# Kernel optimization log

Measured on AMD Instinct MI355X. Metric: run time of the kernel, lower is better.

## Reference

```python
import jax, jax.numpy as jnp
import numpy as np
from jax import lax

N = 200000
CIN = 64
COUT = 128
K = 27  # 3^3 kernel offsets
EPS = 1e-5


def _make_rulebook(key, n, k):
    ki, km = jax.random.split(key)
    idx = jax.random.randint(ki, (k, n), 0, n, dtype=jnp.int32)
    keep = jax.random.uniform(km, (k, n)) < 0.5
    idx = jnp.where(keep, idx, -1)
    # center offset is always the voxel itself (submanifold conv)
    idx = idx.at[k // 2].set(jnp.arange(n, dtype=jnp.int32))
    return idx


def setup_inputs() -> dict:
    key = jax.random.key(0)
    ks = jax.random.split(key, 8)
    feats = jax.random.normal(ks[0], (N, CIN), dtype=jnp.float32)
    nbr1 = _make_rulebook(ks[1], N, K)
    nbr2 = _make_rulebook(ks[2], N, K)
    W1 = jax.random.normal(ks[3], (K, CIN, COUT), dtype=jnp.float32) * 0.05
    W2 = jax.random.normal(ks[4], (K, COUT, COUT), dtype=jnp.float32) * 0.05
    Wd = jax.random.normal(ks[5], (CIN, COUT), dtype=jnp.float32) * 0.05
    g1 = jnp.ones((COUT,), jnp.float32); b1 = jnp.zeros((COUT,), jnp.float32)
    g2 = jnp.ones((COUT,), jnp.float32); b2 = jnp.zeros((COUT,), jnp.float32)
    gd = jnp.ones((COUT,), jnp.float32); bd = jnp.zeros((COUT,), jnp.float32)
    return dict(feats=feats, nbr1=nbr1, nbr2=nbr2, W1=W1, W2=W2, Wd=Wd,
                g1=g1, b1=b1, g2=g2, b2=b2, gd=gd, bd=bd)


def sparse_conv(feats, W, nbr):
    """Rulebook sparse conv: gather neighbors per offset, GEMM, accumulate.
    feats: [N, Cin]; W: [K, Cin, Cout]; nbr: [K, N] int (-1 = missing)."""
    n = feats.shape[0]
    acc0 = jnp.zeros((n, W.shape[-1]), feats.dtype)

    def body(acc, xs):
        idx, Wk = xs  # [N], [Cin, Cout]
        valid = (idx >= 0).astype(feats.dtype)[:, None]
        g = feats[jnp.clip(idx, 0)] * valid  # masked gather [N, Cin]
        return acc + g @ Wk, None

    out, _ = lax.scan(body, acc0, (nbr, W))
    return out


def batchnorm(x, gamma, beta):
    mean = jnp.mean(x, axis=0)
    var = jnp.var(x, axis=0)
    return (x - mean) * lax.rsqrt(var + EPS) * gamma + beta


def reference(feats, nbr1, nbr2, W1, W2, Wd, g1, b1, g2, b2, gd, bd):
    h = sparse_conv(feats, W1, nbr1)
    h = jax.nn.relu(batchnorm(h, g1, b1))
    h = sparse_conv(h, W2, nbr2)
    h = batchnorm(h, g2, b2)
    skip = batchnorm(feats @ Wd, gd, bd)  # 1x1 conv downsample (Cin != Cout)
    return jax.nn.relu(h + skip)
```

## Files before the change

### kernel.cpp

```cpp
#include <hip/hip_runtime.h>
#include <stdint.h>

#define KOFF 27
#define CIN 64
#define COUT 128
#define EPS 1e-5f

using frag_ab = __attribute__((ext_vector_type(8))) short;
using frag_cd = __attribute__((ext_vector_type(4))) float;

__device__ __forceinline__ float bf2f(unsigned short u) {
  union { unsigned int i; float f; } x; x.i = ((unsigned int)u) << 16; return x.f;
}
__device__ __forceinline__ unsigned short f2bf(float f) {
  union { float f; unsigned int i; } x; x.f = f;
  unsigned int u = x.i;
  u += 0x7fffu + ((u >> 16) & 1u);
  return (unsigned short)(u >> 16);
}

__device__ __forceinline__ void gld16(const void* gptr, void* lptr) {
  __builtin_amdgcn_global_load_lds(
      (const __attribute__((address_space(1))) unsigned int*)gptr,
      (__attribute__((address_space(3))) unsigned int*)lptr, 16, 0, 0);
}

template <int CI, bool GATHER, bool OF32>
__global__ __launch_bounds__(256, 3) void conv_kernel(
    const unsigned short* __restrict__ X, const int* __restrict__ nbr,
    const unsigned short* __restrict__ Wt, void* __restrict__ Yv,
    const unsigned short* __restrict__ zpage, float* __restrict__ sums,
    int n, int koff) {
  constexpr int NC = CI / 32;
  __shared__ unsigned short Alds[3][128 * 32];

  const int tid = threadIdx.x;
  const int lane = tid & 63;
  const int wave = tid >> 6;
  const int row0 = blockIdx.x * 128;
  const int wrow = (wave >> 1) * 64;
  const int wcol = (wave & 1) * 64;
  const int m = lane & 15;
  const int q = lane >> 4;
  const int srow0 = wave * 16 + (lane >> 2);
  const int sl = lane & 3;

  frag_cd acc[4][4];
#pragma unroll
  for (int i = 0; i < 4; ++i)
#pragma unroll
    for (int j = 0; j < 4; ++j) acc[i][j] = (frag_cd){0.f, 0.f, 0.f, 0.f};

  frag_ab bA[4], bB[4];
  int idxc[2], idxn[2];

  auto load_idx = [&](int ko, int (&dst)[2]) {
#pragma unroll
    for (int i = 0; i < 2; ++i) {
      const int grow = row0 + srow0 + i * 64;
      int v = -1;
      if (grow < n) v = GATHER ? nbr[(size_t)ko * n + grow] : grow;
      dst[i] = v;
    }
  };
  auto stageA = [&](int buf, int ko, int kc, const int (&idx)[2]) {
#pragma unroll
    for (int i = 0; i < 2; ++i) {
      const int row = srow0 + i * 64;
      const int g = sl ^ ((row >> 1) & 3);
      const unsigned short* ga =
          (idx[i] >= 0) ? X + (size_t)idx[i] * CI + kc * 32 + g * 8 : zpage;
      gld16(ga, &Alds[buf][(i * 64 + wave * 16) * 32]);
    }
  };
  auto loadB = [&](frag_ab (&b)[4], int ko, int kc) {
    const unsigned short* base =
        Wt + (size_t)(ko * NC + kc) * 4096 + q * 1024 + m * 8;
#pragma unroll
    for (int j = 0; j < 4; ++j)
      b[j] = *(const frag_ab*)(base + (wcol + 16 * j) * 8);
  };
  auto do_mfma = [&](int buf, frag_ab (&b)[4]) {
    frag_ab a[4];
#pragma unroll
    for (int i = 0; i < 4; ++i) {
      const int row = wrow + 16 * i + m;
      a[i] = *(const frag_ab*)(&Alds[buf][row * 32 + (q ^ ((row >> 1) & 3)) * 8]);
    }
#pragma unroll
    for (int i = 0; i < 4; ++i)
#pragma unroll
      for (int j = 0; j < 4; ++j)
        acc[i][j] = __builtin_amdgcn_mfma_f32_16x16x32_bf16(a[i], b[j],
                                                            acc[i][j], 0, 0, 0);
  };

  const int T = koff * NC;
  load_idx(0, idxc);
  if (koff > 1) load_idx(1, idxn);
  stageA(0, 0, 0, idxc);
  stageA(1, 0, 1, idxc);
  loadB(bA, 0, 0);

  int bufc = 0;
  auto body = [&](int t, frag_ab (&bcur)[4], frag_ab (&bnxt)[4]) {
    asm volatile("s_waitcnt vmcnt(6)" ::: "memory");
    __builtin_amdgcn_s_barrier();
    const int s = t + 2;
    if (s < T && GATHER) {
      const int kos = s / NC;
      if ((s & (NC - 1)) == 0) {
        idxc[0] = idxn[0];
        idxc[1] = idxn[1];
        if (kos + 1 < koff) load_idx(kos + 1, idxn);
      }
    }
    const int u = t + 1;
    if (u < T) loadB(bnxt, u / NC, u & (NC - 1));
    if (s < T) {
      int bufs = bufc + 2; if (bufs >= 3) bufs -= 3;
      stageA(bufs, s / NC, s & (NC - 1), idxc);
    }
    do_mfma(bufc, bcur);
    if (++bufc == 3) bufc = 0;
  };

  for (int t = 0; t + 3 < T; t += 2) {
    body(t, bA, bB);
    body(t + 1, bB, bA);
  }
  body(T - 2, bA, bB);
  asm volatile("s_waitcnt vmcnt(0)" ::: "memory");
  __builtin_amdgcn_s_barrier();
  do_mfma(bufc, bB);

#pragma unroll
  for (int j = 0; j < 4; ++j) {
    float s = 0.f, qq = 0.f;
#pragma unroll
    for (int i = 0; i < 4; ++i)
#pragma unroll
      for (int r = 0; r < 4; ++r) {
        float v = acc[i][j][r];
        s += v; qq += v * v;
      }
    s += __shfl_xor(s, 16); s += __shfl_xor(s, 32);
    qq += __shfl_xor(qq, 16); qq += __shfl_xor(qq, 32);
    if (lane < 16) {
      const int col = wcol + 16 * j + lane;
      atomicAdd(&sums[col], s);
      atomicAdd(&sums[COUT + col], qq);
    }
  }

#pragma unroll
  for (int i = 0; i < 4; ++i) {
#pragma unroll
    for (int r = 0; r < 4; ++r) {
      const int grow = row0 + wrow + 16 * i + q * 4 + r;
      if (grow < n) {
#pragma unroll
        for (int j = 0; j < 4; ++j) {
          const int gcol = wcol + 16 * j + m;
          if (OF32)
            ((float*)Yv)[(size_t)grow * COUT + gcol] = acc[i][j][r];
          else
            ((unsigned short*)Yv)[(size_t)grow * COUT + gcol] = f2bf(acc[i][j][r]);
        }
      }
    }
  }
}

__global__ __launch_bounds__(256, 2) void convskip_kernel(
    const float* __restrict__ feats, const float* __restrict__ Wd,
    unsigned short* __restrict__ featsb, unsigned short* __restrict__ sX,
    float* __restrict__ sums, int n) {
  __shared__ unsigned short Alds[2][128 * 32];
  const int tid = threadIdx.x;
  const int lane = tid & 63;
  const int wave = tid >> 6;
  const int row0 = blockIdx.x * 128;
  const int wrow = (wave >> 1) * 64;
  const int wcol = (wave & 1) * 64;
  const int m = lane & 15;
  const int q = lane >> 4;

#pragma unroll
  for (int c = 0; c < 4; ++c) {
    int u = c * 256 + tid;
    int kc = u >> 9;
    int v = u & 511;
    int row = v >> 2;
    int s = v & 3;
    int g = s ^ ((row >> 1) & 3);
    int grow = row0 + row;
    uint4 out = make_uint4(0u, 0u, 0u, 0u);
    if (grow < n) {
      const float* p = feats + (size_t)grow * 64 + kc * 32 + g * 8;
      float4 lo = *(const float4*)p;
      float4 hi = *(const float4*)(p + 4);
      out.x = (unsigned)f2bf(lo.x) | ((unsigned)f2bf(lo.y) << 16);
      out.y = (unsigned)f2bf(lo.z) | ((unsigned)f2bf(lo.w) << 16);
      out.z = (unsigned)f2bf(hi.x) | ((unsigned)f2bf(hi.y) << 16);
      out.w = (unsigned)f2bf(hi.z) | ((unsigned)f2bf(hi.w) << 16);
      *(uint4*)(featsb + (size_t)grow * 64 + kc * 32 + g * 8) = out;
    }
    *(uint4*)(&Alds[kc][row * 32 + s * 8]) = out;
  }
  __syncthreads();

  frag_cd acc[4][4];
#pragma unroll
  for (int i = 0; i < 4; ++i)
#pragma unroll
    for (int j = 0; j < 4; ++j) acc[i][j] = (frag_cd){0.f, 0.f, 0.f, 0.f};

#pragma unroll
  for (int kc = 0; kc < 2; ++kc) {
    frag_ab b[4];
#pragma unroll
    for (int j = 0; j < 4; ++j) {
      const int co = wcol + 16 * j + m;
#pragma unroll
      for (int e = 0; e < 8; ++e)
        b[j][e] = (short)f2bf(Wd[(size_t)(kc * 32 + q * 8 + e) * 128 + co]);
    }
    frag_ab a[4];
#pragma unroll
    for (int i = 0; i < 4; ++i) {
      const int row = wrow + 16 * i + m;
      a[i] = *(const frag_ab*)(&Alds[kc][row * 32 + (q ^ ((row >> 1) & 3)) * 8]);
    }
#pragma unroll
    for (int i = 0; i < 4; ++i)
#pragma unroll
      for (int j = 0; j < 4; ++j)
        acc[i][j] = __builtin_amdgcn_mfma_f32_16x16x32_bf16(a[i], b[j],
                                                            acc[i][j], 0, 0, 0);
  }

#pragma unroll
  for (int j = 0; j < 4; ++j) {
    float s = 0.f, qq = 0.f;
#pragma unroll
    for (int i = 0; i < 4; ++i)
#pragma unroll
      for (int r = 0; r < 4; ++r) {
        float v = acc[i][j][r];
        s += v; qq += v * v;
      }
    s += __shfl_xor(s, 16); s += __shfl_xor(s, 32);
    qq += __shfl_xor(qq, 16); qq += __shfl_xor(qq, 32);
    if (lane < 16) {
      const int col = wcol + 16 * j + lane;
      atomicAdd(&sums[col], s);
      atomicAdd(&sums[COUT + col], qq);
    }
  }

#pragma unroll
  for (int i = 0; i < 4; ++i) {
#pragma unroll
    for (int r = 0; r < 4; ++r) {
      const int grow = row0 + wrow + 16 * i + q * 4 + r;
      if (grow < n) {
#pragma unroll
        for (int j = 0; j < 4; ++j)
          sX[(size_t)grow * COUT + wcol + 16 * j + m] = f2bf(acc[i][j][r]);
      }
    }
  }
}

__global__ void prep_kernel(const float* __restrict__ W1,
                            const float* __restrict__ W2,
                            unsigned short* __restrict__ Wt1,
                            unsigned short* __restrict__ Wt2,
                            float* __restrict__ zbase,
                            float* __restrict__ zpage) {
  const int NZ = 768 + 64;
  const int NW1 = KOFF * CIN * 128;
  const int NW2 = KOFF * COUT * 128;
  int gid = blockIdx.x * 256 + threadIdx.x;
  if (gid < NZ) {
    if (gid < 768) zbase[gid] = 0.f; else zpage[gid - 768] = 0.f;
    return;
  }
  gid -= NZ;
  const float* src;
  unsigned short* dst;
  int ci;
  if (gid < NW1) { src = W1; dst = Wt1; ci = CIN; }
  else if (gid < NW1 + NW2) { gid -= NW1; src = W2; dst = Wt2; ci = COUT; }
  else return;
  int e = gid & 7;
  int co = (gid >> 3) & 127;
  int qq = (gid >> 10) & 3;
  int slab = gid >> 12;
  int nc = ci >> 5;
  int ko = slab / nc;
  int kc = slab - ko * nc;
  int cin = kc * 32 + qq * 8 + e;
  dst[gid] = f2bf(src[((size_t)ko * ci + cin) * 128 + co]);
}

__global__ void norm_relu_kernel(unsigned short* __restrict__ x,
                                 const float* __restrict__ sums,
                                 const float* __restrict__ gamma,
                                 const float* __restrict__ beta,
                                 int n, int total8) {
  __shared__ float sc[COUT], sh[COUT];
  const int tid = threadIdx.x;
  if (tid < COUT) {
    float inv_n = 1.f / (float)n;
    float mean = sums[tid] * inv_n;
    float var = sums[COUT + tid] * inv_n - mean * mean;
    float s = gamma[tid] * rsqrtf(var + EPS);
    sc[tid] = s;
    sh[tid] = beta[tid] - mean * s;
  }
  __syncthreads();
  int gid = blockIdx.x * 256 + tid;
  if (gid >= total8) return;
  size_t i = (size_t)gid * 8;
  int c0 = (int)(i & 127);
  uint4 v = *(const uint4*)(x + i);
  unsigned int w[4] = {v.x, v.y, v.z, v.w};
  unsigned int wo[4];
#pragma unroll
  for (int e = 0; e < 4; ++e) {
    int c = c0 + 2 * e;
    float f0 = bf2f((unsigned short)(w[e] & 0xffffu));
    float f1 = bf2f((unsigned short)(w[e] >> 16));
    f0 = fmaxf(f0 * sc[c] + sh[c], 0.f);
    f1 = fmaxf(f1 * sc[c + 1] + sh[c + 1], 0.f);
    wo[e] = (unsigned int)f2bf(f0) | ((unsigned int)f2bf(f1) << 16);
  }
  *(uint4*)(x + i) = make_uint4(wo[0], wo[1], wo[2], wo[3]);
}

__global__ void final_kernel(float* __restrict__ h2,
                             const unsigned short* __restrict__ s,
                             const float* __restrict__ sums2,
                             const float* __restrict__ sumsd,
                             const float* __restrict__ g2,
                             const float* __restrict__ b2,
                             const float* __restrict__ gd,
                             const float* __restrict__ bd,
                             int n, int total4) {
  __shared__ float sc2[COUT], sh2[COUT], scd[COUT], shd[COUT];
  const int tid = threadIdx.x;
  if (tid < COUT) {
    float inv_n = 1.f / (float)n;
    float mean = sums2[tid] * inv_n;
    float var = sums2[COUT + tid] * inv_n - mean * mean;
    float sa = g2[tid] * rsqrtf(var + EPS);
    sc2[tid] = sa;
    sh2[tid] = b2[tid] - mean * sa;
    mean = sumsd[tid] * inv_n;
    var = sumsd[COUT + tid] * inv_n - mean * mean;
    float sb = gd[tid] * rsqrtf(var + EPS);
    scd[tid] = sb;
    shd[tid] = bd[tid] - mean * sb;
  }
  __syncthreads();
  int gid = blockIdx.x * 256 + tid;
  if (gid >= total4) return;
  size_t i = (size_t)gid * 4;
  int c = (int)(i & 127);
  float4 a = *(const float4*)(h2 + i);
  uint2 sv = *(const uint2*)(s + i);
  float b0 = bf2f((unsigned short)(sv.x & 0xffffu));
  float b1 = bf2f((unsigned short)(sv.x >> 16));
  float b2f = bf2f((unsigned short)(sv.y & 0xffffu));
  float b3 = bf2f((unsigned short)(sv.y >> 16));
  float4 o;
  o.x = fmaxf(a.x * sc2[c] + sh2[c] + b0 * scd[c] + shd[c], 0.f);
  o.y = fmaxf(a.y * sc2[c + 1] + sh2[c + 1] + b1 * scd[c + 1] + shd[c + 1], 0.f);
  o.z = fmaxf(a.z * sc2[c + 2] + sh2[c + 2] + b2f * scd[c + 2] + shd[c + 2], 0.f);
  o.w = fmaxf(a.w * sc2[c + 3] + sh2[c + 3] + b3 * scd[c + 3] + shd[c + 3], 0.f);
  *(float4*)(h2 + i) = o;
}

extern "C" void kernel_launch(void* const* d_in, const int* in_sizes, int n_in,
                              void* d_out, int out_size, void* d_ws,
                              size_t ws_size, hipStream_t stream) {
  (void)n_in; (void)out_size; (void)ws_size;
  const float* feats = (const float*)d_in[0];
  const int* nbr1 = (const int*)d_in[1];
  const int* nbr2 = (const int*)d_in[2];
  const float* W1 = (const float*)d_in[3];
  const float* W2 = (const float*)d_in[4];
  const float* Wd = (const float*)d_in[5];
  const float* g1 = (const float*)d_in[6];
  const float* b1 = (const float*)d_in[7];
  const float* g2 = (const float*)d_in[8];
  const float* b2 = (const float*)d_in[9];
  const float* gd = (const float*)d_in[10];
  const float* bd = (const float*)d_in[11];

  const int n = in_sizes[0] / CIN;

  char* ws = (char*)d_ws;
  unsigned short* Wt1 = (unsigned short*)(ws);
  unsigned short* Wt2 = (unsigned short*)(ws + 442368);
  unsigned short* h1 = (unsigned short*)(ws + 1343488);
  unsigned short* sX = (unsigned short*)(ws + 52543488);
  float* sums1 = (float*)(ws + 103743488);
  float* sums2 = sums1 + 2 * COUT;
  float* sumsd = sums1 + 4 * COUT;
  unsigned short* zpage = (unsigned short*)(ws + 103743488 + 8192);

  float* h2 = (float*)d_out;
  unsigned short* featsb = (unsigned short*)((char*)d_out + 76800000);

  const int prep_units = (768 + 64) + KOFF * CIN * 128 + KOFF * COUT * 128;
  prep_kernel<<<(prep_units + 255) / 256, 256, 0, stream>>>(
      W1, W2, Wt1, Wt2, sums1, (float*)zpage);

  const int mblocks = (n + 127) / 128;
  convskip_kernel<<<mblocks, 256, 0, stream>>>(feats, Wd, featsb, sX, sumsd, n);

  conv_kernel<CIN, true, false><<<mblocks, 256, 0, stream>>>(
      featsb, nbr1, Wt1, h1, zpage, sums1, n, KOFF);

  const int total8 = n * COUT / 8;
  norm_relu_kernel<<<(total8 + 255) / 256, 256, 0, stream>>>(h1, sums1, g1, b1, n, total8);

  conv_kernel<COUT, true, true><<<mblocks, 256, 0, stream>>>(
      h1, nbr2, Wt2, h2, zpage, sums2, n, KOFF);

  const int total4 = n * COUT / 4;
  final_kernel<<<(total4 + 255) / 256, 256, 0, stream>>>(
      h2, sX, sums2, sumsd, g2, b2, gd, bd, n, total4);
}
```

Measured before the change: 671.6 us.

## Stage weight tiles through double-buffered LDS via global_load_lds and raise occupancy

Weight fragments were loaded straight from global memory into per-wave registers, with two register sets for double buffering. They are now copied asynchronously into a double-buffered LDS tile with global_load_lds and read from LDS inside the MFMA step. The loop becomes a single unrolled-by-one loop with a tighter vmcnt wait. Launch bounds rise from 3 to 4 blocks per CU. The goal is to cut VGPR pressure and redundant global weight traffic so more blocks fit per CU, at the cost of 16KB more LDS per block and extra LDS reads.

Result: slower. 685.5 us (+2.1%).

```diff
diff --git a/kernel.cpp b/kernel.cpp
--- a/kernel.cpp
+++ b/kernel.cpp
@@ -26,13 +26,14 @@
 }
 
 template <int CI, bool GATHER, bool OF32>
-__global__ __launch_bounds__(256, 3) void conv_kernel(
+__global__ __launch_bounds__(256, 4) void conv_kernel(
     const unsigned short* __restrict__ X, const int* __restrict__ nbr,
     const unsigned short* __restrict__ Wt, void* __restrict__ Yv,
     const unsigned short* __restrict__ zpage, float* __restrict__ sums,
     int n, int koff) {
   constexpr int NC = CI / 32;
   __shared__ unsigned short Alds[3][128 * 32];
+  __shared__ unsigned short Blds[2][4096];
 
   const int tid = threadIdx.x;
   const int lane = tid & 63;
@@ -51,7 +52,6 @@
 #pragma unroll
     for (int j = 0; j < 4; ++j) acc[i][j] = (frag_cd){0.f, 0.f, 0.f, 0.f};
 
-  frag_ab bA[4], bB[4];
   int idxc[2], idxn[2];
 
   auto load_idx = [&](int ko, int (&dst)[2]) {
@@ -63,7 +63,7 @@
       dst[i] = v;
     }
   };
-  auto stageA = [&](int buf, int ko, int kc, const int (&idx)[2]) {
+  auto stageA = [&](int buf, int kc, const int (&idx)[2]) {
 #pragma unroll
     for (int i = 0; i < 2; ++i) {
       const int row = srow0 + i * 64;
@@ -73,20 +73,25 @@
       gld16(ga, &Alds[buf][(i * 64 + wave * 16) * 32]);
     }
   };
-  auto loadB = [&](frag_ab (&b)[4], int ko, int kc) {
-    const unsigned short* base =
-        Wt + (size_t)(ko * NC + kc) * 4096 + q * 1024 + m * 8;
-#pragma unroll
-    for (int j = 0; j < 4; ++j)
-      b[j] = *(const frag_ab*)(base + (wcol + 16 * j) * 8);
+  auto stageB = [&](int buf, int t) {
+    const unsigned short* base = Wt + (size_t)t * 4096;
+#pragma unroll
+    for (int c = 0; c < 2; ++c) {
+      const int chunk = c * 4 + wave;
+      gld16(base + (size_t)chunk * 512 + lane * 8, &Blds[buf][chunk * 512]);
+    }
   };
-  auto do_mfma = [&](int buf, frag_ab (&b)[4]) {
+  auto do_mfma = [&](int abuf, int bbuf) {
     frag_ab a[4];
 #pragma unroll
     for (int i = 0; i < 4; ++i) {
       const int row = wrow + 16 * i + m;
-      a[i] = *(const frag_ab*)(&Alds[buf][row * 32 + (q ^ ((row >> 1) & 3)) * 8]);
-    }
+      a[i] = *(const frag_ab*)(&Alds[abuf][row * 32 + (q ^ ((row >> 1) & 3)) * 8]);
+    }
+    frag_ab b[4];
+#pragma unroll
+    for (int j = 0; j < 4; ++j)
+      b[j] = *(const frag_ab*)(&Blds[bbuf][q * 1024 + (wcol + 16 * j + m) * 8]);
 #pragma unroll
     for (int i = 0; i < 4; ++i)
 #pragma unroll
@@ -98,16 +103,16 @@
   const int T = koff * NC;
   load_idx(0, idxc);
   if (koff > 1) load_idx(1, idxn);
-  stageA(0, 0, 0, idxc);
-  stageA(1, 0, 1, idxc);
-  loadB(bA, 0, 0);
+  stageA(0, 0, idxc);
+  stageB(0, 0);
+  stageA(1, 1, idxc);
 
   int bufc = 0;
-  auto body = [&](int t, frag_ab (&bcur)[4], frag_ab (&bnxt)[4]) {
-    asm volatile("s_waitcnt vmcnt(6)" ::: "memory");
+  for (int t = 0; t < T - 1; ++t) {
+    asm volatile("s_waitcnt vmcnt(2)" ::: "memory");
     __builtin_amdgcn_s_barrier();
     const int s = t + 2;
-    if (s < T && GATHER) {
+    if (GATHER && s < T) {
       const int kos = s / NC;
       if ((s & (NC - 1)) == 0) {
         idxc[0] = idxn[0];
@@ -116,23 +121,17 @@
       }
     }
     const int u = t + 1;
-    if (u < T) loadB(bnxt, u / NC, u & (NC - 1));
+    stageB(u & 1, u);
     if (s < T) {
       int bufs = bufc + 2; if (bufs >= 3) bufs -= 3;
-      stageA(bufs, s / NC, s & (NC - 1), idxc);
-    }
-    do_mfma(bufc, bcur);
+      stageA(bufs, s & (NC - 1), idxc);
+    }
+    do_mfma(bufc, t & 1);
     if (++bufc == 3) bufc = 0;
-  };
-
-  for (int t = 0; t + 3 < T; t += 2) {
-    body(t, bA, bB);
-    body(t + 1, bB, bA);
-  }
-  body(T - 2, bA, bB);
+  }
   asm volatile("s_waitcnt vmcnt(0)" ::: "memory");
   __builtin_amdgcn_s_barrier();
-  do_mfma(bufc, bB);
+  do_mfma(bufc, (T - 1) & 1);
 
 #pragma unroll
   for (int j = 0; j < 4; ++j) {
```

## Load gathered A fragments directly into registers instead of staging through LDS

Applied to the files above, without the earlier changes.

Drops the triple-buffered LDS staging of gathered feature rows, along with its global_load_lds calls and barriers. Each wave now loads its own A fragments straight from global memory into registers and double-buffers them alongside the B fragments. This removes LDS traffic and block-wide synchronisation. In exchange, every row is fetched by both column-half waves, which doubles global gather traffic, and the loop relies on the compiler's waitcnt insertion to hide latency.

Result: slower. 843.1 us (+25.5%).

```diff
diff --git a/kernel.cpp b/kernel.cpp
--- a/kernel.cpp
+++ b/kernel.cpp
@@ -17,12 +17,6 @@
   unsigned int u = x.i;
   u += 0x7fffu + ((u >> 16) & 1u);
   return (unsigned short)(u >> 16);
-}
-
-__device__ __forceinline__ void gld16(const void* gptr, void* lptr) {
-  __builtin_amdgcn_global_load_lds(
-      (const __attribute__((address_space(1))) unsigned int*)gptr,
-      (__attribute__((address_space(3))) unsigned int*)lptr, 16, 0, 0);
 }
 
 template <int CI, bool GATHER, bool OF32>
@@ -32,8 +26,6 @@
     const unsigned short* __restrict__ zpage, float* __restrict__ sums,
     int n, int koff) {
   constexpr int NC = CI / 32;
-  __shared__ unsigned short Alds[3][128 * 32];
-
   const int tid = threadIdx.x;
   const int lane = tid & 63;
   const int wave = tid >> 6;
@@ -42,8 +34,6 @@
   const int wcol = (wave & 1) * 64;
   const int m = lane & 15;
   const int q = lane >> 4;
-  const int srow0 = wave * 16 + (lane >> 2);
-  const int sl = lane & 3;
 
   frag_cd acc[4][4];
 #pragma unroll
@@ -51,42 +41,35 @@
 #pragma unroll
     for (int j = 0; j < 4; ++j) acc[i][j] = (frag_cd){0.f, 0.f, 0.f, 0.f};
 
-  frag_ab bA[4], bB[4];
-  int idxc[2], idxn[2];
-
-  auto load_idx = [&](int ko, int (&dst)[2]) {
-#pragma unroll
-    for (int i = 0; i < 2; ++i) {
-      const int grow = row0 + srow0 + i * 64;
+  frag_ab a0[4], a1[4], b0[4], b1[4];
+  int idxc[4], idxn[4];
+
+  auto load_idx = [&](int ko, int (&dst)[4]) {
+#pragma unroll
+    for (int i = 0; i < 4; ++i) {
+      const int grow = row0 + wrow + 16 * i + m;
       int v = -1;
       if (grow < n) v = GATHER ? nbr[(size_t)ko * n + grow] : grow;
       dst[i] = v;
     }
   };
-  auto stageA = [&](int buf, int ko, int kc, const int (&idx)[2]) {
-#pragma unroll
-    for (int i = 0; i < 2; ++i) {
-      const int row = srow0 + i * 64;
-      const int g = sl ^ ((row >> 1) & 3);
+  auto loadA = [&](frag_ab (&a)[4], int g, const int (&idx)[4]) {
+    const int ch = (g & (NC - 1)) * 32 + q * 8;
+#pragma unroll
+    for (int i = 0; i < 4; ++i) {
       const unsigned short* ga =
-          (idx[i] >= 0) ? X + (size_t)idx[i] * CI + kc * 32 + g * 8 : zpage;
-      gld16(ga, &Alds[buf][(i * 64 + wave * 16) * 32]);
+          (idx[i] >= 0) ? X + (size_t)idx[i] * CI + ch : zpage + q * 8;
+      a[i] = *(const frag_ab*)ga;
     }
   };
-  auto loadB = [&](frag_ab (&b)[4], int ko, int kc) {
+  auto loadB = [&](frag_ab (&b)[4], int g) {
     const unsigned short* base =
-        Wt + (size_t)(ko * NC + kc) * 4096 + q * 1024 + m * 8;
+        Wt + (size_t)g * 4096 + q * 1024 + (wcol << 3) + m * 8;
 #pragma unroll
     for (int j = 0; j < 4; ++j)
-      b[j] = *(const frag_ab*)(base + (wcol + 16 * j) * 8);
+      b[j] = *(const frag_ab*)(base + j * 128);
   };
-  auto do_mfma = [&](int buf, frag_ab (&b)[4]) {
-    frag_ab a[4];
-#pragma unroll
-    for (int i = 0; i < 4; ++i) {
-      const int row = wrow + 16 * i + m;
-      a[i] = *(const frag_ab*)(&Alds[buf][row * 32 + (q ^ ((row >> 1) & 3)) * 8]);
-    }
+  auto mfma16 = [&](frag_ab (&a)[4], frag_ab (&b)[4]) {
 #pragma unroll
     for (int i = 0; i < 4; ++i)
 #pragma unroll
@@ -95,44 +78,33 @@
                                                             acc[i][j], 0, 0, 0);
   };
 
-  const int T = koff * NC;
+  const int G = koff * NC;
+
   load_idx(0, idxc);
+  loadA(a0, 0, idxc);
+  loadB(b0, 0);
   if (koff > 1) load_idx(1, idxn);
-  stageA(0, 0, 0, idxc);
-  stageA(1, 0, 1, idxc);
-  loadB(bA, 0, 0);
-
-  int bufc = 0;
-  auto body = [&](int t, frag_ab (&bcur)[4], frag_ab (&bnxt)[4]) {
-    asm volatile("s_waitcnt vmcnt(6)" ::: "memory");
-    __builtin_amdgcn_s_barrier();
-    const int s = t + 2;
-    if (s < T && GATHER) {
-      const int kos = s / NC;
-      if ((s & (NC - 1)) == 0) {
-        idxc[0] = idxn[0];
-        idxc[1] = idxn[1];
-        if (kos + 1 < koff) load_idx(kos + 1, idxn);
+
+  auto body = [&](int g, frag_ab (&ca)[4], frag_ab (&cb)[4],
+                  frag_ab (&na)[4], frag_ab (&nb)[4]) {
+    const int u = g + 1;
+    if (u < G) {
+      if ((u & (NC - 1)) == 0) {
+        const int kou = u / NC;
+#pragma unroll
+        for (int c = 0; c < 4; ++c) idxc[c] = idxn[c];
+        if (kou + 1 < koff) load_idx(kou + 1, idxn);
       }
-    }
-    const int u = t + 1;
-    if (u < T) loadB(bnxt, u / NC, u & (NC - 1));
-    if (s < T) {
-      int bufs = bufc + 2; if (bufs >= 3) bufs -= 3;
-      stageA(bufs, s / NC, s & (NC - 1), idxc);
-    }
-    do_mfma(bufc, bcur);
-    if (++bufc == 3) bufc = 0;
+      loadA(na, u, idxc);
+      loadB(nb, u);
+    }
+    mfma16(ca, cb);
   };
 
-  for (int t = 0; t + 3 < T; t += 2) {
-    body(t, bA, bB);
-    body(t + 1, bB, bA);
-  }
-  body(T - 2, bA, bB);
-  asm volatile("s_waitcnt vmcnt(0)" ::: "memory");
-  __builtin_amdgcn_s_barrier();
-  do_mfma(bufc, bB);
+  for (int g = 0; g < G; g += 2) {
+    body(g, a0, b0, a1, b1);
+    body(g + 1, a1, b1, a0, b0);
+  }
 
 #pragma unroll
   for (int j = 0; j < 4; ++j) {
```
